# Kernel tuning notes

Hardware: AMD Instinct MI355X
Metric: run time of the kernel (lower is better)

## Reference

```python
import jax, jax.numpy as jnp
import numpy as np

EPS = 1e-6
QMAX = 127.0  # hif8 emulated as symmetric 8-bit fake-quant (true hif8 numerics are proprietary)


def _rotate_half(v):
    d = v.shape[-1] // 2
    return jnp.concatenate([-v[..., d:], v[..., :d]], axis=-1)


def _quant(v):
    # per-row (last-axis) absmax quantization emulating hif8 with a per-tensor-row scale
    amax = jnp.max(jnp.abs(v), axis=-1, keepdims=True)
    scale = jnp.maximum(amax / QMAX, 1e-8)
    q = jnp.round(v / scale)
    return q, jnp.squeeze(scale, -1)


def setup_inputs() -> dict:
    key = jax.random.key(0)
    ks = jax.random.split(key, 16)
    B, S, H, Hn, D, L = 2, 4096, 2048, 32, 128, 16384
    return {
        "x": jax.random.normal(ks[0], (B, S, H), jnp.float32),
        "q_norm": jax.random.uniform(ks[1], (H,), jnp.float32),
        "q_norm_scale": jax.random.uniform(ks[2], (H,), jnp.float32),
        "w_qb": jax.random.normal(ks[3], (H, Hn * D), jnp.float32),
        "w_qb_scale": jax.random.uniform(ks[4], (Hn * D,), jnp.float32),
        "wk": jax.random.normal(ks[5], (H, D), jnp.float32),
        "w_proj": jax.random.normal(ks[6], (H, Hn), jnp.float32),
        "ln_gamma_k": jax.random.uniform(ks[7], (H,), jnp.float32),
        "ln_beta_k": jax.random.normal(ks[8], (H,), jnp.float32),
        "cos_idx_rope": jax.random.uniform(ks[9], (S, D), jnp.float32),
        "sin_idx_rope": jax.random.uniform(ks[10], (S, D), jnp.float32),
        "hadamard_q": jax.random.normal(ks[11], (D, D), jnp.float32),
        "hadamard_k": jax.random.normal(ks[12], (D, D), jnp.float32),
        "k_cache": jnp.zeros((L, D), jnp.float32),
        "k_cache_scale": jnp.zeros((L,), jnp.float32),
        "k_cache_index": jnp.arange(B * S, dtype=jnp.int32).reshape(B, S),
    }


def reference(x, q_norm, q_norm_scale, w_qb, w_qb_scale, wk, w_proj,
              ln_gamma_k, ln_beta_k, cos_idx_rope, sin_idx_rope,
              hadamard_q, hadamard_k, k_cache, k_cache_scale, k_cache_index):
    B, S, H = x.shape
    D = hadamard_q.shape[0]
    Hn = w_qb.shape[1] // D

    # ---- Q branch: RMSNorm + smooth scale -> quantized GEMM (dequant fused) ----
    rms = jax.lax.rsqrt(jnp.mean(x * x, axis=-1, keepdims=True) + EPS)
    xq = x * rms * q_norm * q_norm_scale                      # [B,S,H]
    q = jnp.einsum('bsh,hd->bsd', xq, w_qb) * w_qb_scale      # [B,S,Hn*D]
    q = q.reshape(B, S, Hn, D)

    cos_q = cos_idx_rope[:S][None, :, None, :]
    sin_q = sin_idx_rope[:S][None, :, None, :]
    q = q * cos_q + _rotate_half(q) * sin_q                   # RoPE
    q = jnp.einsum('bshd,de->bshe', q, hadamard_q)            # Hadamard mix
    q_hif8, q_scale = _quant(q)                               # [B,S,Hn,D], [B,S,Hn]

    # ---- K branch: LayerNorm -> proj -> RoPE -> Hadamard -> quant ----
    mu = jnp.mean(x, axis=-1, keepdims=True)
    var = jnp.mean(jnp.square(x - mu), axis=-1, keepdims=True)
    xk = (x - mu) * jax.lax.rsqrt(var + EPS) * ln_gamma_k + ln_beta_k
    k = jnp.einsum('bsh,hd->bsd', xk, wk)                     # [B,S,D]
    cos_k = cos_idx_rope[:S][None, :, :]
    sin_k = sin_idx_rope[:S][None, :, :]
    k = k * cos_k + _rotate_half(k) * sin_k
    k = jnp.einsum('bsd,de->bse', k, hadamard_k)
    k_q, k_s = _quant(k)                                      # [B,S,D], [B,S]

    # ---- scatter quantized K into the indexer cache ----
    idx = k_cache_index.reshape(-1)
    k_hif8 = k_cache.at[idx].set(k_q.reshape(-1, D))
    k_scale = k_cache_scale.at[idx].set(k_s.reshape(-1))

    # ---- per-head indexer weights ----
    weights = jnp.einsum('bsh,he->bse', x, w_proj)            # [B,S,Hn]

    return (q_hif8, q_scale, k_hif8, k_scale, weights)
```

## Files before the change

kernel.cpp:

```cpp
#include <hip/hip_runtime.h>
#include <hip/hip_bf16.h>
#include <stdint.h>

constexpr int Mrows = 8192;
constexpr int Hdim  = 2048;
constexpr int Sdim  = 4096;
constexpr int HnD   = 4096;
constexpr int Hn    = 32;
constexpr int Dd    = 128;
constexpr int Lc    = 16384;
constexpr int NFULL = 4352;

typedef unsigned short u16;
typedef __attribute__((ext_vector_type(8))) short    bf16x8;
typedef __attribute__((ext_vector_type(4))) float    f32x4;
typedef __attribute__((ext_vector_type(8))) unsigned short u16x8;

__device__ __forceinline__ float bf2f(u16 u) {
    union { unsigned int i; float f; } v; v.i = ((unsigned int)u) << 16; return v.f;
}
__device__ __forceinline__ u16 f2bf(float f) {
    union { float f; unsigned int i; } v; v.f = f;
    unsigned int x = v.i;
    return (u16)((x + 0x7fffu + ((x >> 16) & 1u)) >> 16);
}
__device__ __forceinline__ void gload_lds16(const void* g, void* l) {
    __builtin_amdgcn_global_load_lds(
        (const __attribute__((address_space(1))) void*)g,
        (__attribute__((address_space(3))) void*)l, 16, 0, 0);
}

__global__ __launch_bounds__(256) void stats_cvt(
    const float* __restrict__ x, u16* __restrict__ xb, float* __restrict__ rms,
    float* __restrict__ mu, float* __restrict__ rstd)
{
    int r = blockIdx.x, t = threadIdx.x;
    const float4* xr = (const float4*)(x + (size_t)r * Hdim);
    float4 a = xr[2 * t], bq = xr[2 * t + 1];
    float v[8] = {a.x, a.y, a.z, a.w, bq.x, bq.y, bq.z, bq.w};
    float s = 0.f, ss = 0.f;
    __align__(16) u16 o[8];
    #pragma unroll
    for (int i = 0; i < 8; i++) { s += v[i]; ss += v[i] * v[i]; o[i] = f2bf(v[i]); }
    ((u16x8*)(xb + (size_t)r * Hdim))[t] = *(const u16x8*)o;
    for (int oo = 32; oo > 0; oo >>= 1) { s += __shfl_down(s, oo); ss += __shfl_down(ss, oo); }
    __shared__ float as[4], ass[4];
    if ((t & 63) == 0) { as[t >> 6] = s; ass[t >> 6] = ss; }
    __syncthreads();
    if (t == 0) {
        float S1 = as[0] + as[1] + as[2] + as[3];
        float S2 = ass[0] + ass[1] + ass[2] + ass[3];
        float mean = S1 / Hdim, msq = S2 / Hdim;
        rms[r]  = rsqrtf(msq + 1e-6f);
        mu[r]   = mean;
        rstd[r] = rsqrtf(msq - mean * mean + 1e-6f);
    }
}

__global__ __launch_bounds__(256) void prep_wt(
    const float* __restrict__ wqb, const float* __restrict__ qn, const float* __restrict__ qns,
    const float* __restrict__ wk,  const float* __restrict__ g,  const float* __restrict__ wproj,
    u16* __restrict__ wt)
{
    __shared__ u16 tile[64][72];
    int k0 = blockIdx.x * 64, n0 = blockIdx.y * 64;
    int t = threadIdx.x;
    int lk = t >> 2, lc0 = (t & 3) * 16;
    int k = k0 + lk;
    float c1k = qn[k] * qns[k];
    float gk  = g[k];
    #pragma unroll
    for (int i = 0; i < 16; i++) {
        int n = n0 + lc0 + i;
        float val;
        if (n < 4096)      val = wqb[(size_t)k * HnD + n] * c1k;
        else if (n < 4224) val = wk[k * Dd + (n - 4096)] * gk;
        else if (n < 4256) val = wproj[k * Hn + (n - 4224)];
        else               val = 0.f;
        tile[lk][lc0 + i] = f2bf(val);
    }
    __syncthreads();
    int ln = t >> 2, lk0 = (t & 3) * 16;
    __align__(16) u16 o[16];
    #pragma unroll
    for (int i = 0; i < 16; i++) o[i] = tile[lk0 + i][ln];
    u16* dst = wt + (size_t)(n0 + ln) * Hdim + k0 + lk0;
    *(u16x8*)dst = *(const u16x8*)o;
    *(u16x8*)(dst + 8) = *((const u16x8*)o + 1);
}

__global__ __launch_bounds__(256) void transpose_h(
    const float* __restrict__ hq, const float* __restrict__ hk,
    u16* __restrict__ hqt, u16* __restrict__ hkt)
{
    __shared__ float tile[128][129];
    const float* src = blockIdx.x ? hk : hq;
    u16* dst = blockIdx.x ? hkt : hqt;
    int t = threadIdx.x;
    int r = t >> 1, h = (t & 1) * 64;
    #pragma unroll
    for (int j = 0; j < 16; j++) {
        float4 v = *(const float4*)(src + r * Dd + h + 4 * j);
        tile[r][h + 4 * j]     = v.x;
        tile[r][h + 4 * j + 1] = v.y;
        tile[r][h + 4 * j + 2] = v.z;
        tile[r][h + 4 * j + 3] = v.w;
    }
    __syncthreads();
    #pragma unroll
    for (int j0 = 0; j0 < 64; j0 += 8) {
        __align__(16) u16 o[8];
        #pragma unroll
        for (int j = 0; j < 8; j++) o[j] = f2bf(tile[h + j0 + j][r]);
        *(u16x8*)(dst + r * Dd + h + j0) = *(const u16x8*)o;
    }
}

__global__ __launch_bounds__(256) void bg_dot(
    const float* __restrict__ wk, const float* __restrict__ g, const float* __restrict__ b,
    float* __restrict__ bdot, float* __restrict__ gdot)
{
    int n = blockIdx.x, t = threadIdx.x;
    float sb = 0.f, sg = 0.f;
    for (int k = t; k < Hdim; k += 256) {
        float w = wk[k * Dd + n];
        sb += b[k] * w;
        sg += g[k] * w;
    }
    for (int o = 32; o > 0; o >>= 1) { sb += __shfl_down(sb, o); sg += __shfl_down(sg, o); }
    __shared__ float rb[4], rg[4];
    if ((t & 63) == 0) { rb[t >> 6] = sb; rg[t >> 6] = sg; }
    __syncthreads();
    if (t == 0) { bdot[n] = rb[0] + rb[1] + rb[2] + rb[3]; gdot[n] = rg[0] + rg[1] + rg[2] + rg[3]; }
}

__global__ __launch_bounds__(256) void main_gemm(
    const u16* __restrict__ A, const u16* __restrict__ Bt,
    const float* __restrict__ rms, const float* __restrict__ mu, const float* __restrict__ rstd,
    const float* __restrict__ qbs,
    const float* __restrict__ bdot, const float* __restrict__ gdot,
    const u16* __restrict__ hqt,
    const float* __restrict__ cosr, const float* __restrict__ sinr,
    float* __restrict__ oq,
    float* __restrict__ oqs,
    float* __restrict__ kpre,
    float* __restrict__ wout)
{
    constexpr int BK = 32;
    constexpr int PB = 272;
    __shared__ __align__(16) char lds[128 * PB];
    u16* smA = (u16*)lds;
    u16* smB = (u16*)(lds + 8192);

    int bm = blockIdx.x, bn = blockIdx.y;
    int tid = threadIdx.x, w = tid >> 6, lane = tid & 63;
    int quad = lane >> 4, l15 = lane & 15;
    int brow = bm * 128;

    f32x4 acc[2][8] = {};

    const int srow = w * 32 + (lane >> 2);
    const int kch  = (lane & 3) * 8;
    const u16* Ab = A  + (size_t)brow * Hdim;
    const u16* Bb = Bt + (size_t)(bn * 128) * Hdim;

    for (int k0 = 0; k0 < Hdim; k0 += BK) {
        __syncthreads();
        #pragma unroll
        for (int c = 0; c < 2; c++) {
            int r = srow + c * 16;
            gload_lds16(Ab + (size_t)r * Hdim + k0 + kch, smA + (w * 32 + c * 16) * BK);
            gload_lds16(Bb + (size_t)r * Hdim + k0 + kch, smB + (w * 32 + c * 16) * BK);
        }
        __syncthreads();
        bf16x8 af[2], bfq[8];
        #pragma unroll
        for (int mt = 0; mt < 2; mt++)
            af[mt] = *(const bf16x8*)(smA + (w * 32 + mt * 16 + l15) * BK + quad * 8);
        #pragma unroll
        for (int nt = 0; nt < 8; nt++)
            bfq[nt] = *(const bf16x8*)(smB + (nt * 16 + l15) * BK + quad * 8);
        #pragma unroll
        for (int mt = 0; mt < 2; mt++)
            #pragma unroll
            for (int nt = 0; nt < 8; nt++)
                acc[mt][nt] = __builtin_amdgcn_mfma_f32_16x16x32_bf16(af[mt], bfq[nt], acc[mt][nt], 0, 0, 0);
    }

    if (bn < 32) {
        __syncthreads();
        float qb[8];
        #pragma unroll
        for (int nt = 0; nt < 8; nt++) qb[nt] = qbs[bn * 128 + nt * 16 + l15];
        #pragma unroll
        for (int mt = 0; mt < 2; mt++) {
            float y[8][4];
            #pragma unroll
            for (int reg = 0; reg < 4; reg++) {
                float rv = rms[brow + w * 32 + mt * 16 + quad * 4 + reg];
                #pragma unroll
                for (int nt = 0; nt < 8; nt++) y[nt][reg] = acc[mt][nt][reg] * rv * qb[nt];
            }
            #pragma unroll
            for (int reg = 0; reg < 4; reg++) {
                int rl = w * 32 + mt * 16 + quad * 4 + reg;
                int s_ = (brow + rl) & (Sdim - 1);
                const float* cr = cosr + (size_t)s_ * Dd + l15;
                const float* sr = sinr + (size_t)s_ * Dd + l15;
                u16* prow = (u16*)(lds + rl * PB);
                #pragma unroll
                for (int nt = 0; nt < 8; nt++) {
                    float c  = cr[nt * 16];
                    float sv = sr[nt * 16];
                    float sign = (nt < 4) ? -1.f : 1.f;
                    float o = y[nt][reg] * c + sign * y[nt ^ 4][reg] * sv;
                    prow[nt * 16 + l15] = f2bf(o);
                }
            }
        }
        __syncthreads();
        f32x4 a2[2][8] = {};
        #pragma unroll
        for (int kb = 0; kb < 4; kb++) {
            bf16x8 pa[2];
            #pragma unroll
            for (int mt = 0; mt < 2; mt++)
                pa[mt] = *(const bf16x8*)(lds + (w * 32 + mt * 16 + l15) * PB + kb * 64 + quad * 16);
            #pragma unroll
            for (int nt = 0; nt < 8; nt++) {
                bf16x8 hb = *(const bf16x8*)(hqt + (size_t)(nt * 16 + l15) * Dd + kb * 32 + quad * 8);
                #pragma unroll
                for (int mt = 0; mt < 2; mt++)
                    a2[mt][nt] = __builtin_amdgcn_mfma_f32_16x16x32_bf16(pa[mt], hb, a2[mt][nt], 0, 0, 0);
            }
        }
        #pragma unroll
        for (int mt = 0; mt < 2; mt++)
            #pragma unroll
            for (int reg = 0; reg < 4; reg++) {
                float m = 0.f;
                #pragma unroll
                for (int nt = 0; nt < 8; nt++) m = fmaxf(m, fabsf(a2[mt][nt][reg]));
                m = fmaxf(m, __shfl_xor(m, 8));
                m = fmaxf(m, __shfl_xor(m, 4));
                m = fmaxf(m, __shfl_xor(m, 2));
                m = fmaxf(m, __shfl_xor(m, 1));
                float scale = fmaxf(m * (1.f / 127.f), 1e-8f);
                float inv = 1.f / scale;
                int r = brow + w * 32 + mt * 16 + quad * 4 + reg;
                float* orow = oq + (size_t)r * HnD + bn * 128;
                #pragma unroll
                for (int nt = 0; nt < 8; nt++)
                    orow[nt * 16 + l15] = rintf(a2[mt][nt][reg] * inv);
                if (l15 == 0) oqs[(size_t)r * Hn + bn] = scale;
            }
    } else if (bn == 32) {
        float bd[8], gd[8];
        #pragma unroll
        for (int nt = 0; nt < 8; nt++) { bd[nt] = bdot[nt * 16 + l15]; gd[nt] = gdot[nt * 16 + l15]; }
        #pragma unroll
        for (int mt = 0; mt < 2; mt++)
            #pragma unroll
            for (int reg = 0; reg < 4; reg++) {
                int r = brow + w * 32 + mt * 16 + quad * 4 + reg;
                float sd = rstd[r], m_ = mu[r];
                #pragma unroll
                for (int nt = 0; nt < 8; nt++)
                    kpre[(size_t)r * Dd + nt * 16 + l15] = acc[mt][nt][reg] * sd + bd[nt] - sd * m_ * gd[nt];
            }
    } else {
        #pragma unroll
        for (int mt = 0; mt < 2; mt++)
            #pragma unroll
            for (int reg = 0; reg < 4; reg++) {
                int r = brow + w * 32 + mt * 16 + quad * 4 + reg;
                #pragma unroll
                for (int nt = 0; nt < 2; nt++)
                    wout[(size_t)r * Hn + nt * 16 + l15] = acc[mt][nt][reg];
            }
    }
}

__global__ void copy_cache(const float* __restrict__ kc, const float* __restrict__ kcs,
                           float* __restrict__ dk, float* __restrict__ dks)
{
    int g = blockIdx.x * 256 + threadIdx.x;
    ((float4*)dk)[2 * g]     = ((const float4*)kc)[2 * g];
    ((float4*)dk)[2 * g + 1] = ((const float4*)kc)[2 * g + 1];
    if (g < Lc / 8) {
        ((float4*)dks)[2 * g]     = ((const float4*)kcs)[2 * g];
        ((float4*)dks)[2 * g + 1] = ((const float4*)kcs)[2 * g + 1];
    }
}

template <int IS_K>
__global__ __launch_bounds__(256) void post_kernel(
    const float* src,
    const u16* __restrict__ ht,
    const float* __restrict__ cosr, const float* __restrict__ sinr,
    const int* __restrict__ idx,
    float* dstq, float* __restrict__ dsts)
{
    constexpr int RP = 136;
    __shared__ __align__(16) u16 sA[32 * RP];
    __shared__ __align__(16) u16 sB[128 * RP];
    __shared__ float pamax[32][2];
    __shared__ int sidx[32];

    int blk = blockIdx.x, tid = threadIdx.x;

    {
        int n = tid >> 1, kk0 = (tid & 1) * 64;
        const u16x8* gp = (const u16x8*)(ht + n * Dd + kk0);
        u16* lb = sB + n * RP + kk0;
        #pragma unroll
        for (int j = 0; j < 8; j++) *(u16x8*)(lb + j * 8) = gp[j];
    }
    {
        int r = tid >> 3, c = tid & 7;
        int d0 = c * 16;
        int s_ = IS_K ? ((blk * 32 + r) & (Sdim - 1)) : (blk & (Sdim - 1));
        const float* srow = src + (size_t)blk * 4096 + r * Dd;
        int p0 = (d0 + 64) & 127;
        float sign = (d0 < 64) ? -1.f : 1.f;
        float vv[16], pv[16], cv[16], sv[16];
        #pragma unroll
        for (int j = 0; j < 4; j++) {
            float4 a = *(const float4*)(srow + d0 + 4 * j);
            float4 p = *(const float4*)(srow + p0 + 4 * j);
            float4 cc = *(const float4*)(cosr + (size_t)s_ * Dd + d0 + 4 * j);
            float4 sc = *(const float4*)(sinr + (size_t)s_ * Dd + d0 + 4 * j);
            vv[4*j] = a.x; vv[4*j+1] = a.y; vv[4*j+2] = a.z; vv[4*j+3] = a.w;
            pv[4*j] = p.x; pv[4*j+1] = p.y; pv[4*j+2] = p.z; pv[4*j+3] = p.w;
            cv[4*j] = cc.x; cv[4*j+1] = cc.y; cv[4*j+2] = cc.z; cv[4*j+3] = cc.w;
            sv[4*j] = sc.x; sv[4*j+1] = sc.y; sv[4*j+2] = sc.z; sv[4*j+3] = sc.w;
        }
        __align__(16) u16 o[16];
        #pragma unroll
        for (int i = 0; i < 16; i++)
            o[i] = f2bf(vv[i] * cv[i] + sign * pv[i] * sv[i]);
        u16* la = sA + r * RP + d0;
        *(u16x8*)la = *(const u16x8*)o;
        *(u16x8*)(la + 8) = *((const u16x8*)o + 1);
        if (IS_K && tid < 32) sidx[tid] = idx[blk * 32 + tid];
    }
    __syncthreads();

    int w = tid >> 6, lane = tid & 63, quad = lane >> 4, l15 = lane & 15;
    int rs = (w & 1) * 16, cg = (w >> 1) * 64;
    f32x4 acc[4] = {};
    #pragma unroll
    for (int kb = 0; kb < 4; kb++) {
        bf16x8 a = *(const bf16x8*)(sA + (rs + l15) * RP + kb * 32 + quad * 8);
        #pragma unroll
        for (int nt = 0; nt < 4; nt++) {
            bf16x8 b = *(const bf16x8*)(sB + (cg + nt * 16 + l15) * RP + kb * 32 + quad * 8);
            acc[nt] = __builtin_amdgcn_mfma_f32_16x16x32_bf16(a, b, acc[nt], 0, 0, 0);
        }
    }
    #pragma unroll
    for (int reg = 0; reg < 4; reg++) {
        float m = 0.f;
        #pragma unroll
        for (int nt = 0; nt < 4; nt++) m = fmaxf(m, fabsf(acc[nt][reg]));
        m = fmaxf(m, __shfl_xor(m, 8));
        m = fmaxf(m, __shfl_xor(m, 4));
        m = fmaxf(m, __shfl_xor(m, 2));
        m = fmaxf(m, __shfl_xor(m, 1));
        if (l15 == 0) pamax[rs + quad * 4 + reg][w >> 1] = m;
    }
    __syncthreads();
    #pragma unroll
    for (int reg = 0; reg < 4; reg++) {
        int r = rs + quad * 4 + reg;
        float am = fmaxf(pamax[r][0], pamax[r][1]);
        float scale = fmaxf(am * (1.f / 127.f), 1e-8f);
        float inv = 1.f / scale;
        size_t dro = IS_K ? (size_t)sidx[r] * Dd : (size_t)blk * 4096 + (size_t)r * Dd;
        #pragma unroll
        for (int nt = 0; nt < 4; nt++)
            dstq[dro + cg + nt * 16 + l15] = rintf(acc[nt][reg] * inv);
        if (l15 == 0 && (w >> 1) == 0)
            dsts[IS_K ? sidx[r] : blk * Hn + r] = scale;
    }
}

extern "C" void kernel_launch(void* const* d_in, const int* in_sizes, int n_in,
                              void* d_out, int out_size, void* d_ws, size_t ws_size,
                              hipStream_t stream) {
    (void)in_sizes; (void)n_in; (void)out_size; (void)ws_size;
    const float* x    = (const float*)d_in[0];
    const float* qn   = (const float*)d_in[1];
    const float* qns  = (const float*)d_in[2];
    const float* wqb  = (const float*)d_in[3];
    const float* wqbs = (const float*)d_in[4];
    const float* wk   = (const float*)d_in[5];
    const float* wpj  = (const float*)d_in[6];
    const float* g    = (const float*)d_in[7];
    const float* b    = (const float*)d_in[8];
    const float* cosr = (const float*)d_in[9];
    const float* sinr = (const float*)d_in[10];
    const float* hq   = (const float*)d_in[11];
    const float* hk   = (const float*)d_in[12];
    const float* kc   = (const float*)d_in[13];
    const float* kcs  = (const float*)d_in[14];
    const int*   idx  = (const int*)d_in[15];

    char* ws = (char*)d_ws;
    size_t o = 0;
    u16* xb  = (u16*)(ws + o); o += (size_t)Mrows * Hdim * 2;
    u16* wt  = (u16*)(ws + o); o += (size_t)NFULL * Hdim * 2;
    u16* hqt = (u16*)(ws + o); o += Dd * Dd * 2;
    u16* hkt = (u16*)(ws + o); o += Dd * Dd * 2;
    float* rmsb  = (float*)(ws + o); o += (size_t)Mrows * 4;
    float* mub   = (float*)(ws + o); o += (size_t)Mrows * 4;
    float* rstdb = (float*)(ws + o); o += (size_t)Mrows * 4;
    float* bdotb = (float*)(ws + o); o += 512;
    float* gdotb = (float*)(ws + o); o += 512;
    float* kpre  = (float*)(ws + o); o += (size_t)Mrows * Dd * 4;

    float* out = (float*)d_out;
    float* oq  = out;
    float* oqs = oq  + (size_t)Mrows * HnD;
    float* ok  = oqs + (size_t)Mrows * Hn;
    float* oks = ok  + (size_t)Lc * Dd;
    float* ow  = oks + Lc;

    stats_cvt<<<Mrows, 256, 0, stream>>>(x, xb, rmsb, mub, rstdb);
    prep_wt<<<dim3(Hdim / 64, NFULL / 64), 256, 0, stream>>>(wqb, qn, qns, wk, g, wpj, wt);
    transpose_h<<<2, 256, 0, stream>>>(hq, hk, hqt, hkt);
    bg_dot<<<Dd, 256, 0, stream>>>(wk, g, b, bdotb, gdotb);
    main_gemm<<<dim3(Mrows / 128, NFULL / 128), 256, 0, stream>>>(
        xb, wt, rmsb, mub, rstdb, wqbs, bdotb, gdotb, hqt, cosr, sinr, oq, oqs, kpre, ow);
    copy_cache<<<(Lc * Dd / 8) / 256, 256, 0, stream>>>(kc, kcs, ok, oks);
    post_kernel<1><<<Mrows / 32, 256, 0, stream>>>(kpre, hkt, cosr, sinr, idx, ok, oks);
}
```

Measured before the change: 554.7 us.

## Rewrite main GEMM with 256x256 tiles, double-buffered swizzled LDS and XCD-aware block mapping

The fused GEMM moves from 128x128 tiles with BK=32 and a sync-load-compute loop to 256x256 tiles with 512 threads and BK=64. Global-to-LDS loads are double-buffered and prefetched while MFMAs run, with an XOR swizzle to avoid LDS bank conflicts, plus setprio and sched barriers. The block index is remapped so tiles are grouped per XCD for L2 reuse. The epilogue is adapted so each wave pair handles one head, and the K/weights tile is split by wave column. This raises arithmetic intensity and overlaps memory with compute, at the cost of 128KB LDS per block and high register pressure.

```diff
diff --git a/kernel.cpp b/kernel.cpp
--- a/kernel.cpp
+++ b/kernel.cpp
@@ -134,150 +134,210 @@
     if (t == 0) { bdot[n] = rb[0] + rb[1] + rb[2] + rb[3]; gdot[n] = rg[0] + rg[1] + rg[2] + rg[3]; }
 }
 
-__global__ __launch_bounds__(256) void main_gemm(
+#define LDA_(buf, mt, kk) (*(const bf16x8*)(lds + (buf)*65536 + \
+    (wr*64 + (mt)*16 + l15) * 128 + ((((kk)*4 + quad) ^ (l15 & 7)) * 16)))
+#define LDB_(buf, nt, kk) (*(const bf16x8*)(lds + (buf)*65536 + 32768 + \
+    (wc*128 + (nt)*16 + l15) * 128 + ((((kk)*4 + quad) ^ (l15 & 7)) * 16)))
+#define STAGE_A(buf, g, kt) gload_lds16( \
+    Ab + (size_t)((g)*64 + r64) * Hdim + (kt)*64 + cswz, \
+    ldst + (buf)*65536 + (g)*8192)
+#define STAGE_B(buf, g, kt) gload_lds16( \
+    Bb + (size_t)((g)*64 + r64) * Hdim + (kt)*64 + cswz, \
+    ldst + (buf)*65536 + 32768 + (g)*8192)
+
+__global__ __launch_bounds__(512, 2) void main_gemm(
     const u16* __restrict__ A, const u16* __restrict__ Bt,
     const float* __restrict__ rms, const float* __restrict__ mu, const float* __restrict__ rstd,
     const float* __restrict__ qbs,
     const float* __restrict__ bdot, const float* __restrict__ gdot,
     const u16* __restrict__ hqt,
     const float* __restrict__ cosr, const float* __restrict__ sinr,
-    float* __restrict__ oq,
-    float* __restrict__ oqs,
-    float* __restrict__ kpre,
-    float* __restrict__ wout)
-{
-    constexpr int BK = 32;
-    constexpr int PB = 272;
-    __shared__ __align__(16) char lds[128 * PB];
-    u16* smA = (u16*)lds;
-    u16* smB = (u16*)(lds + 8192);
-
-    int bm = blockIdx.x, bn = blockIdx.y;
-    int tid = threadIdx.x, w = tid >> 6, lane = tid & 63;
-    int quad = lane >> 4, l15 = lane & 15;
-    int brow = bm * 128;
-
-    f32x4 acc[2][8] = {};
-
-    const int srow = w * 32 + (lane >> 2);
-    const int kch  = (lane & 3) * 8;
+    float* __restrict__ oq, float* __restrict__ oqs,
+    float* __restrict__ kpre, float* __restrict__ wout)
+{
+    __shared__ __align__(16) char lds[131072];
+
+    int tid = threadIdx.x;
+    int w = tid >> 6, lane = tid & 63, quad = lane >> 4, l15 = lane & 15;
+    int wr = w >> 1, wc = w & 1;
+    int lin = blockIdx.x + 32 * blockIdx.y;
+    int wg = (lin & 7) * 68 + (lin >> 3);
+    int bm = wg & 31, bn = wg >> 5;
+    int brow = bm * 256;
+
     const u16* Ab = A  + (size_t)brow * Hdim;
-    const u16* Bb = Bt + (size_t)(bn * 128) * Hdim;
-
-    for (int k0 = 0; k0 < Hdim; k0 += BK) {
+    const u16* Bb = Bt + (size_t)(bn * 256) * Hdim;
+
+    int r64 = tid >> 3;
+    int cswz = (((tid & 7) ^ (r64 & 7)) * 8);
+    char* ldst = lds + (tid >> 6) * 1024;
+
+    f32x4 acc[4][8] = {};
+
+    #pragma unroll
+    for (int g = 0; g < 4; g++) { STAGE_A(0, g, 0); STAGE_B(0, g, 0); }
+
+    for (int t = 0; t < 32; t++) {
+        int buf = t & 1, nb = buf ^ 1;
+        bool pf = (t + 1 < 32);
+        asm volatile("s_waitcnt vmcnt(0)" ::: "memory");
+        __builtin_amdgcn_sched_barrier(0);
+        __builtin_amdgcn_s_barrier();
+
+        bf16x8 a0[4], a1[4], bfr[4];
+        #pragma unroll
+        for (int mt = 0; mt < 4; mt++) a0[mt] = LDA_(buf, mt, 0);
+        #pragma unroll
+        for (int nt = 0; nt < 4; nt++) bfr[nt] = LDB_(buf, nt, 0);
+        if (pf) { STAGE_A(nb, 0, t+1); STAGE_A(nb, 1, t+1); STAGE_A(nb, 2, t+1); STAGE_A(nb, 3, t+1); }
+        asm volatile("s_waitcnt lgkmcnt(0)" ::: "memory");
+        __builtin_amdgcn_sched_barrier(0);
+        __builtin_amdgcn_s_setprio(1);
+        #pragma unroll
+        for (int mt = 0; mt < 4; mt++)
+            #pragma unroll
+            for (int nt = 0; nt < 4; nt++)
+                acc[mt][nt] = __builtin_amdgcn_mfma_f32_16x16x32_bf16(a0[mt], bfr[nt], acc[mt][nt], 0, 0, 0);
+        __builtin_amdgcn_s_setprio(0);
+        __builtin_amdgcn_s_barrier();
+        #pragma unroll
+        for (int nt = 0; nt < 4; nt++) bfr[nt] = LDB_(buf, 4 + nt, 0);
+        if (pf) { STAGE_B(nb, 0, t+1); STAGE_B(nb, 1, t+1); STAGE_B(nb, 2, t+1); STAGE_B(nb, 3, t+1); }
+        asm volatile("s_waitcnt lgkmcnt(0)" ::: "memory");
+        __builtin_amdgcn_sched_barrier(0);
+        __builtin_amdgcn_s_setprio(1);
+        #pragma unroll
+        for (int mt = 0; mt < 4; mt++)
+            #pragma unroll
+            for (int nt = 0; nt < 4; nt++)
+                acc[mt][4 + nt] = __builtin_amdgcn_mfma_f32_16x16x32_bf16(a0[mt], bfr[nt], acc[mt][4 + nt], 0, 0, 0);
+        __builtin_amdgcn_s_setprio(0);
+        __builtin_amdgcn_s_barrier();
+        #pragma unroll
+        for (int mt = 0; mt < 4; mt++) a1[mt] = LDA_(buf, mt, 1);
+        #pragma unroll
+        for (int nt = 0; nt < 4; nt++) bfr[nt] = LDB_(buf, nt, 1);
+        asm volatile("s_waitcnt lgkmcnt(0)" ::: "memory");
+        __builtin_amdgcn_sched_barrier(0);
+        __builtin_amdgcn_s_setprio(1);
+        #pragma unroll
+        for (int mt = 0; mt < 4; mt++)
+            #pragma unroll
+            for (int nt = 0; nt < 4; nt++)
+                acc[mt][nt] = __builtin_amdgcn_mfma_f32_16x16x32_bf16(a1[mt], bfr[nt], acc[mt][nt], 0, 0, 0);
+        __builtin_amdgcn_s_setprio(0);
+        __builtin_amdgcn_s_barrier();
+        #pragma unroll
+        for (int nt = 0; nt < 4; nt++) bfr[nt] = LDB_(buf, 4 + nt, 1);
+        asm volatile("s_waitcnt lgkmcnt(0)" ::: "memory");
+        __builtin_amdgcn_sched_barrier(0);
+        __builtin_amdgcn_s_setprio(1);
+        #pragma unroll
+        for (int mt = 0; mt < 4; mt++)
+            #pragma unroll
+            for (int nt = 0; nt < 4; nt++)
+                acc[mt][4 + nt] = __builtin_amdgcn_mfma_f32_16x16x32_bf16(a1[mt], bfr[nt], acc[mt][4 + nt], 0, 0, 0);
+        __builtin_amdgcn_s_setprio(0);
+        __builtin_amdgcn_s_barrier();
+    }
+
+    if (bn < 16) {
         __syncthreads();
-        #pragma unroll
-        for (int c = 0; c < 2; c++) {
-            int r = srow + c * 16;
-            gload_lds16(Ab + (size_t)r * Hdim + k0 + kch, smA + (w * 32 + c * 16) * BK);
-            gload_lds16(Bb + (size_t)r * Hdim + k0 + kch, smB + (w * 32 + c * 16) * BK);
-        }
-        __syncthreads();
-        bf16x8 af[2], bfq[8];
-        #pragma unroll
-        for (int mt = 0; mt < 2; mt++)
-            af[mt] = *(const bf16x8*)(smA + (w * 32 + mt * 16 + l15) * BK + quad * 8);
-        #pragma unroll
-        for (int nt = 0; nt < 8; nt++)
-            bfq[nt] = *(const bf16x8*)(smB + (nt * 16 + l15) * BK + quad * 8);
-        #pragma unroll
-        for (int mt = 0; mt < 2; mt++)
-            #pragma unroll
-            for (int nt = 0; nt < 8; nt++)
-                acc[mt][nt] = __builtin_amdgcn_mfma_f32_16x16x32_bf16(af[mt], bfq[nt], acc[mt][nt], 0, 0, 0);
-    }
-
-    if (bn < 32) {
-        __syncthreads();
+        int head = bn * 2 + wc;
+        char* Pw = lds + w * 16384;
         float qb[8];
         #pragma unroll
-        for (int nt = 0; nt < 8; nt++) qb[nt] = qbs[bn * 128 + nt * 16 + l15];
-        #pragma unroll
-        for (int mt = 0; mt < 2; mt++) {
+        for (int nt = 0; nt < 8; nt++) qb[nt] = qbs[head * 128 + nt * 16 + l15];
+        #pragma unroll
+        for (int mt = 0; mt < 4; mt++) {
             float y[8][4];
             #pragma unroll
             for (int reg = 0; reg < 4; reg++) {
-                float rv = rms[brow + w * 32 + mt * 16 + quad * 4 + reg];
+                float rv = rms[brow + wr * 64 + mt * 16 + quad * 4 + reg];
                 #pragma unroll
                 for (int nt = 0; nt < 8; nt++) y[nt][reg] = acc[mt][nt][reg] * rv * qb[nt];
             }
             #pragma unroll
             for (int reg = 0; reg < 4; reg++) {
-                int rl = w * 32 + mt * 16 + quad * 4 + reg;
-                int s_ = (brow + rl) & (Sdim - 1);
+                int rp = mt * 16 + quad * 4 + reg;
+                int s_ = (brow + wr * 64 + rp) & (Sdim - 1);
                 const float* cr = cosr + (size_t)s_ * Dd + l15;
                 const float* sr = sinr + (size_t)s_ * Dd + l15;
-                u16* prow = (u16*)(lds + rl * PB);
+                int sw = (rp & 7) << 4;
                 #pragma unroll
                 for (int nt = 0; nt < 8; nt++) {
                     float c  = cr[nt * 16];
                     float sv = sr[nt * 16];
                     float sign = (nt < 4) ? -1.f : 1.f;
                     float o = y[nt][reg] * c + sign * y[nt ^ 4][reg] * sv;
-                    prow[nt * 16 + l15] = f2bf(o);
+                    int colb = (nt * 16 + l15) * 2;
+                    *(u16*)(Pw + rp * 256 + (colb ^ sw)) = f2bf(o);
                 }
             }
         }
         __syncthreads();
-        f32x4 a2[2][8] = {};
-        #pragma unroll
-        for (int kb = 0; kb < 4; kb++) {
-            bf16x8 pa[2];
-            #pragma unroll
-            for (int mt = 0; mt < 2; mt++)
-                pa[mt] = *(const bf16x8*)(lds + (w * 32 + mt * 16 + l15) * PB + kb * 64 + quad * 16);
+        #pragma unroll
+        for (int mt = 0; mt < 4; mt++) {
+            bf16x8 pa[4];
+            #pragma unroll
+            for (int kb = 0; kb < 4; kb++) {
+                int row = mt * 16 + l15;
+                pa[kb] = *(const bf16x8*)(Pw + row * 256 + ((kb * 64 + quad * 16) ^ ((row & 7) << 4)));
+            }
+            f32x4 a2[8] = {};
             #pragma unroll
             for (int nt = 0; nt < 8; nt++) {
-                bf16x8 hb = *(const bf16x8*)(hqt + (size_t)(nt * 16 + l15) * Dd + kb * 32 + quad * 8);
-                #pragma unroll
-                for (int mt = 0; mt < 2; mt++)
-                    a2[mt][nt] = __builtin_amdgcn_mfma_f32_16x16x32_bf16(pa[mt], hb, a2[mt][nt], 0, 0, 0);
+                #pragma unroll
+                for (int kb = 0; kb < 4; kb++) {
+                    bf16x8 hb = *(const bf16x8*)(hqt + (size_t)(nt * 16 + l15) * Dd + kb * 32 + quad * 8);
+                    a2[nt] = __builtin_amdgcn_mfma_f32_16x16x32_bf16(pa[kb], hb, a2[nt], 0, 0, 0);
+                }
             }
-        }
-        #pragma unroll
-        for (int mt = 0; mt < 2; mt++)
             #pragma unroll
             for (int reg = 0; reg < 4; reg++) {
                 float m = 0.f;
                 #pragma unroll
-                for (int nt = 0; nt < 8; nt++) m = fmaxf(m, fabsf(a2[mt][nt][reg]));
+                for (int nt = 0; nt < 8; nt++) m = fmaxf(m, fabsf(a2[nt][reg]));
                 m = fmaxf(m, __shfl_xor(m, 8));
                 m = fmaxf(m, __shfl_xor(m, 4));
                 m = fmaxf(m, __shfl_xor(m, 2));
                 m = fmaxf(m, __shfl_xor(m, 1));
                 float scale = fmaxf(m * (1.f / 127.f), 1e-8f);
                 float inv = 1.f / scale;
-                int r = brow + w * 32 + mt * 16 + quad * 4 + reg;
-                float* orow = oq + (size_t)r * HnD + bn * 128;
+                int r = brow + wr * 64 + mt * 16 + quad * 4 + reg;
+                float* orow = oq + (size_t)r * HnD + head * 128;
                 #pragma unroll
                 for (int nt = 0; nt < 8; nt++)
-                    orow[nt * 16 + l15] = rintf(a2[mt][nt][reg] * inv);
-                if (l15 == 0) oqs[(size_t)r * Hn + bn] = scale;
+                    orow[nt * 16 + l15] = rintf(a2[nt][reg] * inv);
+                if (l15 == 0) oqs[(size_t)r * Hn + head] = scale;
             }
-    } else if (bn == 32) {
-        float bd[8], gd[8];
-        #pragma unroll
-        for (int nt = 0; nt < 8; nt++) { bd[nt] = bdot[nt * 16 + l15]; gd[nt] = gdot[nt * 16 + l15]; }
-        #pragma unroll
-        for (int mt = 0; mt < 2; mt++)
-            #pragma unroll
-            for (int reg = 0; reg < 4; reg++) {
-                int r = brow + w * 32 + mt * 16 + quad * 4 + reg;
-                float sd = rstd[r], m_ = mu[r];
-                #pragma unroll
-                for (int nt = 0; nt < 8; nt++)
-                    kpre[(size_t)r * Dd + nt * 16 + l15] = acc[mt][nt][reg] * sd + bd[nt] - sd * m_ * gd[nt];
-            }
+        }
     } else {
-        #pragma unroll
-        for (int mt = 0; mt < 2; mt++)
-            #pragma unroll
-            for (int reg = 0; reg < 4; reg++) {
-                int r = brow + w * 32 + mt * 16 + quad * 4 + reg;
-                #pragma unroll
-                for (int nt = 0; nt < 2; nt++)
-                    wout[(size_t)r * Hn + nt * 16 + l15] = acc[mt][nt][reg];
-            }
+        if (wc == 0) {
+            float bd[8], gd[8];
+            #pragma unroll
+            for (int nt = 0; nt < 8; nt++) { bd[nt] = bdot[nt * 16 + l15]; gd[nt] = gdot[nt * 16 + l15]; }
+            #pragma unroll
+            for (int mt = 0; mt < 4; mt++)
+                #pragma unroll
+                for (int reg = 0; reg < 4; reg++) {
+                    int r = brow + wr * 64 + mt * 16 + quad * 4 + reg;
+                    float sd = rstd[r], m_ = mu[r];
+                    #pragma unroll
+                    for (int nt = 0; nt < 8; nt++)
+                        kpre[(size_t)r * Dd + nt * 16 + l15] = acc[mt][nt][reg] * sd + bd[nt] - sd * m_ * gd[nt];
+                }
+        } else {
+            #pragma unroll
+            for (int mt = 0; mt < 4; mt++)
+                #pragma unroll
+                for (int reg = 0; reg < 4; reg++) {
+                    int r = brow + wr * 64 + mt * 16 + quad * 4 + reg;
+                    #pragma unroll
+                    for (int nt = 0; nt < 2; nt++)
+                        wout[(size_t)r * Hn + nt * 16 + l15] = acc[mt][nt][reg];
+                }
+        }
     }
 }
 
@@ -430,7 +490,7 @@
     prep_wt<<<dim3(Hdim / 64, NFULL / 64), 256, 0, stream>>>(wqb, qn, qns, wk, g, wpj, wt);
     transpose_h<<<2, 256, 0, stream>>>(hq, hk, hqt, hkt);
     bg_dot<<<Dd, 256, 0, stream>>>(wk, g, b, bdotb, gdotb);
-    main_gemm<<<dim3(Mrows / 128, NFULL / 128), 256, 0, stream>>>(
+    main_gemm<<<dim3(32, 17), 512, 0, stream>>>(
         xb, wt, rmsb, mub, rstdb, wqbs, bdotb, gdotb, hqt, cosr, sinr, oq, oqs, kpre, ow);
     copy_cache<<<(Lc * Dd / 8) / 256, 256, 0, stream>>>(kc, kcs, ok, oks);
     post_kernel<1><<<Mrows / 32, 256, 0, stream>>>(kpre, hkt, cosr, sinr, idx, ok, oks);
```

After: 525.2 us. -5.3%, faster.
